# Kernel optimization log

Measured on AMD Instinct MI355X. Metric: run time of the kernel, lower is better.

Reference implementation:

```python
import jax, jax.numpy as jnp
import numpy as np

B, LQ, LK, D, H = 8, 1024, 1024, 1024, 16
HD = D // H  # 64


def setup_inputs() -> dict:
    key = jax.random.key(0)
    ks = jax.random.split(key, 8)
    s = 0.02  # weight init scale
    return {
        "q_in": jax.random.normal(ks[0], (B, LQ, D), jnp.float32),
        "k_in": jax.random.normal(ks[1], (B, LK, D), jnp.float32),
        "v_in": jax.random.normal(ks[2], (B, LK, D), jnp.float32),
        "wq": jax.random.normal(ks[3], (D, D), jnp.float32) * s,
        "bq": jnp.zeros((D,), jnp.float32),
        "wk": jax.random.normal(ks[4], (D, D), jnp.float32) * s,
        "bk": jnp.zeros((D,), jnp.float32),
        "wv": jax.random.normal(ks[5], (D, D), jnp.float32) * s,
        "bv": jnp.zeros((D,), jnp.float32),
        "wo": jax.random.normal(ks[6], (D, D), jnp.float32) * s,
        "bo": jnp.zeros((D,), jnp.float32),
        # is_masked=True buffer: tril of ones -> True on lower triangle (masked-out positions, per original masked_fill semantics)
        "mask": jnp.tril(jnp.ones((LQ, LK), jnp.bool_)),
    }


def reference(q_in, k_in, v_in, wq, bq, wk, bk, wv, bv, wo, bo, mask):
    # torch Linear: x @ W.T + b
    q = (q_in @ wq.T + bq).reshape(B, H, LQ, HD)  # plain view, as in original
    k = (k_in @ wk.T + bk).reshape(B, H, LK, HD)
    v = (v_in @ wv.T + bv).reshape(B, H, LK, HD)
    # QUIRK: original scales by sqrt(query.size(1)) == sqrt(head_num), not sqrt(head_dim)
    scale = jnp.sqrt(jnp.float32(H))
    h = jnp.einsum("bhik,bhjk->bhij", q, k) / scale  # [B,H,LQ,LK]
    # masked_fill(-inf) then nan_to_num (maps -inf -> finfo.min, matching torch defaults)
    h = jnp.nan_to_num(jnp.where(mask, -jnp.inf, h))
    w = jax.nn.softmax(h, axis=-1)
    heads = jnp.einsum("bhij,bhjv->bhiv", w, v).reshape(B, LQ, H * HD)
    return heads @ wo.T + bo
```

## Files before the change

kernel.cpp:

```cpp
#include <hip/hip_runtime.h>
#include <hip/hip_bf16.h>

typedef __bf16 bf16;
typedef _Float16 f16;
typedef __attribute__((ext_vector_type(8))) __bf16 bf16x8;
typedef __attribute__((ext_vector_type(4))) __bf16 bf16x4;
typedef __attribute__((ext_vector_type(8))) _Float16 f16x8;
typedef __attribute__((ext_vector_type(4))) _Float16 f16x4;
typedef __attribute__((ext_vector_type(4))) float f32x4;

#define BB 8
#define SEQ 1024
#define DD 1024
#define HDIM 64
#define CHUNK 65536
#define MROWS (BB * SEQ)
#define NE_IN 8388608
#define NE_W  1048576

#define QSCALE 0.3606737602222409f

__device__ __forceinline__ void async_load16(const bf16* g, bf16* l) {
  __builtin_amdgcn_global_load_lds(
      (const __attribute__((address_space(1))) void*)g,
      (__attribute__((address_space(3))) void*)l, 16, 0, 0);
}

struct CvtArgs {
  const float* src[7];
  bf16* dst[7];
  int n[7];
};
__global__ __launch_bounds__(256) void cvt_bf16(CvtArgs a) {
  const int t = blockIdx.y;
  const long idx = ((long)blockIdx.x * 256 + threadIdx.x) * 8;
  if (idx >= a.n[t]) return;
  const float* s = a.src[t] + idx;
  f32x4 x = *(const f32x4*)s;
  f32x4 y = *(const f32x4*)(s + 4);
  bf16x8 o;
  o[0] = (bf16)x[0]; o[1] = (bf16)x[1]; o[2] = (bf16)x[2]; o[3] = (bf16)x[3];
  o[4] = (bf16)y[0]; o[5] = (bf16)y[1]; o[6] = (bf16)y[2]; o[7] = (bf16)y[3];
  *(bf16x8*)(a.dst[t] + idx) = o;
}

__global__ __launch_bounds__(256) void gemm_qkv(
    const bf16* __restrict__ Abase, const bf16* __restrict__ Wbase,
    const float* __restrict__ bq, const float* __restrict__ bk,
    const float* __restrict__ bv, bf16* __restrict__ Obase)
{
  __shared__ __attribute__((aligned(16))) bf16 As[128 * 32];
  __shared__ __attribute__((aligned(16))) bf16 Bs[128 * 32];

  const int tid  = threadIdx.x;
  const int lane = tid & 63;
  const int wid  = tid >> 6;
  const int wm   = wid >> 1, wn = wid & 1;
  const int quad = lane >> 4, l15 = lane & 15;
  const int m0 = blockIdx.x * 128;
  const int n0 = blockIdx.y * 128;
  const int t  = n0 >> 10;

  const bf16* A = Abase + (size_t)t * NE_IN;
  const float* bias = (t == 0) ? bq : (t == 1) ? bk : bv;
  const float scale = (t == 0) ? QSCALE : 1.0f;
  bf16* Cout = Obase + (size_t)t * NE_IN;
  const int nc0 = n0 & 1023;

  f32x4 acc[4][4];
#pragma unroll
  for (int i = 0; i < 4; i++)
#pragma unroll
    for (int j = 0; j < 4; j++) acc[i][j] = f32x4{0.f, 0.f, 0.f, 0.f};

  const int srow = wid * 16 + (lane >> 2);
  const int scol = (lane & 3) * 8;
  const bf16* gA = A + (size_t)(m0 + srow) * DD + scol;
  const bf16* gB = Wbase + (size_t)(n0 + srow) * DD + scol;
  bf16* lA = As + wid * 512;
  bf16* lB = Bs + wid * 512;

  for (int k0 = 0; k0 < DD; k0 += 32) {
    async_load16(gA + k0,           lA);
    async_load16(gA + k0 + 64 * DD, lA + 2048);
    async_load16(gB + k0,           lB);
    async_load16(gB + k0 + 64 * DD, lB + 2048);
    __syncthreads();

    bf16x8 af[4], bfr[4];
#pragma unroll
    for (int mi = 0; mi < 4; mi++)
      af[mi] = *(const bf16x8*)&As[(wm * 64 + mi * 16 + l15) * 32 + quad * 8];
#pragma unroll
    for (int ni = 0; ni < 4; ni++)
      bfr[ni] = *(const bf16x8*)&Bs[(wn * 64 + ni * 16 + l15) * 32 + quad * 8];
#pragma unroll
    for (int mi = 0; mi < 4; mi++)
#pragma unroll
      for (int ni = 0; ni < 4; ni++)
        acc[mi][ni] = __builtin_amdgcn_mfma_f32_16x16x32_bf16(
            af[mi], bfr[ni], acc[mi][ni], 0, 0, 0);
    __syncthreads();
  }

#pragma unroll
  for (int mi = 0; mi < 4; mi++) {
#pragma unroll
    for (int ni = 0; ni < 4; ni++) {
      const int col = nc0 + wn * 64 + ni * 16 + l15;
      const float bv_ = bias[col];
#pragma unroll
      for (int r = 0; r < 4; r++) {
        const int row = m0 + wm * 64 + mi * 16 + quad * 4 + r;
        Cout[(size_t)row * DD + col] = (bf16)((acc[mi][ni][r] + bv_) * scale);
      }
    }
  }
}

__global__ __launch_bounds__(256) void gemm_out(
    const bf16* __restrict__ A, const bf16* __restrict__ Bw,
    const float* __restrict__ bias, float* __restrict__ Cout)
{
  __shared__ __attribute__((aligned(16))) bf16 As[128 * 32];
  __shared__ __attribute__((aligned(16))) bf16 Bs[128 * 32];

  const int tid  = threadIdx.x;
  const int lane = tid & 63;
  const int wid  = tid >> 6;
  const int wm   = wid >> 1, wn = wid & 1;
  const int quad = lane >> 4, l15 = lane & 15;
  const int m0 = blockIdx.x * 128;
  const int n0 = blockIdx.y * 128;

  f32x4 acc[4][4];
#pragma unroll
  for (int i = 0; i < 4; i++)
#pragma unroll
    for (int j = 0; j < 4; j++) acc[i][j] = f32x4{0.f, 0.f, 0.f, 0.f};

  const int srow = wid * 16 + (lane >> 2);
  const int scol = (lane & 3) * 8;
  const bf16* gA = A  + (size_t)(m0 + srow) * DD + scol;
  const bf16* gB = Bw + (size_t)(n0 + srow) * DD + scol;
  bf16* lA = As + wid * 512;
  bf16* lB = Bs + wid * 512;

  for (int k0 = 0; k0 < DD; k0 += 32) {
    async_load16(gA + k0,           lA);
    async_load16(gA + k0 + 64 * DD, lA + 2048);
    async_load16(gB + k0,           lB);
    async_load16(gB + k0 + 64 * DD, lB + 2048);
    __syncthreads();

    bf16x8 af[4], bfr[4];
#pragma unroll
    for (int mi = 0; mi < 4; mi++)
      af[mi] = *(const bf16x8*)&As[(wm * 64 + mi * 16 + l15) * 32 + quad * 8];
#pragma unroll
    for (int ni = 0; ni < 4; ni++)
      bfr[ni] = *(const bf16x8*)&Bs[(wn * 64 + ni * 16 + l15) * 32 + quad * 8];
#pragma unroll
    for (int mi = 0; mi < 4; mi++)
#pragma unroll
      for (int ni = 0; ni < 4; ni++)
        acc[mi][ni] = __builtin_amdgcn_mfma_f32_16x16x32_bf16(
            af[mi], bfr[ni], acc[mi][ni], 0, 0, 0);
    __syncthreads();
  }

#pragma unroll
  for (int mi = 0; mi < 4; mi++) {
#pragma unroll
    for (int ni = 0; ni < 4; ni++) {
      const int col = n0 + wn * 64 + ni * 16 + l15;
      const float bv_ = bias[col];
#pragma unroll
      for (int r = 0; r < 4; r++) {
        const int row = m0 + wm * 64 + mi * 16 + quad * 4 + r;
        Cout[(size_t)row * DD + col] = acc[mi][ni][r] + bv_;
      }
    }
  }
}

__global__ __launch_bounds__(256) void vtrans(
    const bf16* __restrict__ V, f16* __restrict__ Vt)
{
  __shared__ __attribute__((aligned(16))) bf16 T[64][72];
  const int tid = threadIdx.x;
  const int r  = tid >> 2;
  const int c0 = (tid & 3) * 16;
  const size_t base = (size_t)blockIdx.y * CHUNK;
  const int kv0 = blockIdx.x * 64;

  const bf16* src = V + base + (size_t)(kv0 + r) * HDIM + c0;
  *(bf16x8*)&T[r][c0]     = *(const bf16x8*)src;
  *(bf16x8*)&T[r][c0 + 8] = *(const bf16x8*)(src + 8);
  __syncthreads();

  f16x8 o0, o1;
#pragma unroll
  for (int j = 0; j < 8; j++) {
    o0[j] = (f16)(float)T[c0 + j][r];
    o1[j] = (f16)(float)T[c0 + 8 + j][r];
  }
  f16* dst = Vt + base + (size_t)r * SEQ + kv0 + c0;
  *(f16x8*)dst       = o0;
  *(f16x8*)(dst + 8) = o1;
}

__global__ __launch_bounds__(256) void attn6(
    const bf16* __restrict__ Q, const bf16* __restrict__ K,
    const f16* __restrict__ Vt, bf16* __restrict__ O)
{
  __shared__ __attribute__((aligned(16))) bf16 Ks[64][72];
  __shared__ __attribute__((aligned(16))) f16  Vs[64][72];

  const int tid  = threadIdx.x;
  const int lane = tid & 63;
  const int wid  = tid >> 6;
  const int quad = lane >> 4, l15 = lane & 15;
  const int q0   = blockIdx.y * 128;
  const size_t base = (size_t)blockIdx.x * CHUNK;

  const int sA = q0 + wid * 16;
  const int sB = sA + 64;
  const int qgA = sA + l15;
  const int qgB = sB + l15;

  bf16x8 qbA[2], qbB[2];
#pragma unroll
  for (int ks = 0; ks < 2; ks++) {
    qbA[ks] = *(const bf16x8*)&Q[base + (size_t)qgA * HDIM + ks * 32 + quad * 8];
    qbB[ks] = *(const bf16x8*)&Q[base + (size_t)qgB * HDIM + ks * 32 + quad * 8];
  }

  f32x4 oaccA[4], oaccB[4], laccA, laccB;
#pragma unroll
  for (int h = 0; h < 4; h++) {
    oaccA[h] = f32x4{0.f, 0.f, 0.f, 0.f};
    oaccB[h] = f32x4{0.f, 0.f, 0.f, 0.f};
  }
  laccA = f32x4{0.f, 0.f, 0.f, 0.f};
  laccB = f32x4{0.f, 0.f, 0.f, 0.f};
  const f16x4 ones = f16x4{(f16)1.f, (f16)1.f, (f16)1.f, (f16)1.f};

  const int sr = tid >> 2;
  const int sc = (tid & 3) * 16;
  const bf16* gK = K  + base + (size_t)sr * HDIM + sc;
  const f16*  gV = Vt + base + (size_t)sr * SEQ  + sc;

  const bool lastBlk = (q0 == SEQ - 128);
  const int kv_begin = lastBlk ? 0 : q0;
  const bool uniRow = lastBlk && (wid == 3);

  for (int kv0 = kv_begin; kv0 < SEQ; kv0 += 64) {
    {
      const bf16* pk = gK + (size_t)kv0 * HDIM;
      *(bf16x8*)&Ks[sr][sc]     = *(const bf16x8*)pk;
      *(bf16x8*)&Ks[sr][sc + 8] = *(const bf16x8*)(pk + 8);
      const f16* pv = gV + kv0;
      *(f16x8*)&Vs[sr][sc]     = *(const f16x8*)pv;
      *(f16x8*)&Vs[sr][sc + 8] = *(const f16x8*)(pv + 8);
    }
    __syncthreads();

    const bool activeA = (kv0 + 63 > sA);
    const bool activeB = (kv0 + 63 > sB);

#pragma unroll
    for (int t = 0; t < 4; t++) {
      bf16x8 kf0 = *(const bf16x8*)&Ks[t * 16 + l15][quad * 8];
      bf16x8 kf1 = *(const bf16x8*)&Ks[t * 16 + l15][32 + quad * 8];
      f16x4 vf[4];
#pragma unroll
      for (int h = 0; h < 4; h++)
        vf[h] = *(const f16x4*)&Vs[h * 16 + l15][t * 16 + quad * 4];

      if (activeA) {
        f32x4 s = f32x4{0.f, 0.f, 0.f, 0.f};
        s = __builtin_amdgcn_mfma_f32_16x16x32_bf16(kf0, qbA[0], s, 0, 0, 0);
        s = __builtin_amdgcn_mfma_f32_16x16x32_bf16(kf1, qbA[1], s, 0, 0, 0);
        f16x4 pf;
        if (kv0 + t * 16 <= sA + 15) {
#pragma unroll
          for (int r = 0; r < 4; r++) {
            const int kvg = kv0 + t * 16 + quad * 4 + r;
            const float p = (kvg <= qgA) ? 0.f : __builtin_amdgcn_exp2f(s[r]);
            pf[r] = (f16)p;
          }
        } else {
#pragma unroll
          for (int r = 0; r < 4; r++) pf[r] = (f16)__builtin_amdgcn_exp2f(s[r]);
        }
        laccA = __builtin_amdgcn_mfma_f32_16x16x16f16(ones, pf, laccA, 0, 0, 0);
#pragma unroll
        for (int h = 0; h < 4; h++)
          oaccA[h] = __builtin_amdgcn_mfma_f32_16x16x16f16(vf[h], pf, oaccA[h], 0, 0, 0);
      }

      if (activeB) {
        f32x4 s = f32x4{0.f, 0.f, 0.f, 0.f};
        s = __builtin_amdgcn_mfma_f32_16x16x32_bf16(kf0, qbB[0], s, 0, 0, 0);
        s = __builtin_amdgcn_mfma_f32_16x16x32_bf16(kf1, qbB[1], s, 0, 0, 0);
        f16x4 pf;
        if (kv0 + t * 16 <= sB + 15) {
#pragma unroll
          for (int r = 0; r < 4; r++) {
            const int kvg = kv0 + t * 16 + quad * 4 + r;
            const float p = (kvg <= qgB) ? ((qgB == SEQ - 1) ? 1.f : 0.f)
                                         : __builtin_amdgcn_exp2f(s[r]);
            pf[r] = (f16)p;
          }
        } else {
#pragma unroll
          for (int r = 0; r < 4; r++) pf[r] = (f16)__builtin_amdgcn_exp2f(s[r]);
        }
        laccB = __builtin_amdgcn_mfma_f32_16x16x16f16(ones, pf, laccB, 0, 0, 0);
#pragma unroll
        for (int h = 0; h < 4; h++)
          oaccB[h] = __builtin_amdgcn_mfma_f32_16x16x16f16(vf[h], pf, oaccB[h], 0, 0, 0);
      } else if (uniRow) {
        f16x4 pf = (l15 == 15) ? ones : f16x4{(f16)0.f, (f16)0.f, (f16)0.f, (f16)0.f};
        laccB = __builtin_amdgcn_mfma_f32_16x16x16f16(ones, pf, laccB, 0, 0, 0);
#pragma unroll
        for (int h = 0; h < 4; h++)
          oaccB[h] = __builtin_amdgcn_mfma_f32_16x16x16f16(vf[h], pf, oaccB[h], 0, 0, 0);
      }
    }
    __syncthreads();
  }

  const float rinvA = 1.0f / laccA[0];
  const float rinvB = 1.0f / laccB[0];

#pragma unroll
  for (int h = 0; h < 4; h++) {
    bf16x4 w;
#pragma unroll
    for (int r = 0; r < 4; r++) w[r] = (bf16)(oaccA[h][r] * rinvA);
    *(bf16x4*)&Ks[wid * 16 + l15][h * 16 + quad * 4] = w;
  }
  __syncthreads();
  {
    const int row = tid >> 2;
    const int c   = (tid & 3) * 16;
    bf16* dst = O + base + (size_t)(q0 + row) * HDIM + c;
    *(bf16x8*)dst       = *(const bf16x8*)&Ks[row][c];
    *(bf16x8*)(dst + 8) = *(const bf16x8*)&Ks[row][c + 8];
  }
  __syncthreads();
#pragma unroll
  for (int h = 0; h < 4; h++) {
    bf16x4 w;
#pragma unroll
    for (int r = 0; r < 4; r++) w[r] = (bf16)(oaccB[h][r] * rinvB);
    *(bf16x4*)&Ks[wid * 16 + l15][h * 16 + quad * 4] = w;
  }
  __syncthreads();
  {
    const int row = tid >> 2;
    const int c   = (tid & 3) * 16;
    bf16* dst = O + base + (size_t)(q0 + 64 + row) * HDIM + c;
    *(bf16x8*)dst       = *(const bf16x8*)&Ks[row][c];
    *(bf16x8*)(dst + 8) = *(const bf16x8*)&Ks[row][c + 8];
  }
}

extern "C" void kernel_launch(void* const* d_in, const int* in_sizes, int n_in,
                              void* d_out, int out_size, void* d_ws, size_t ws_size,
                              hipStream_t stream) {
  (void)in_sizes; (void)n_in; (void)out_size; (void)ws_size;
  const float* q_in = (const float*)d_in[0];
  const float* k_in = (const float*)d_in[1];
  const float* v_in = (const float*)d_in[2];
  const float* wq   = (const float*)d_in[3];
  const float* bq   = (const float*)d_in[4];
  const float* wk   = (const float*)d_in[5];
  const float* bk   = (const float*)d_in[6];
  const float* wv   = (const float*)d_in[7];
  const float* bv   = (const float*)d_in[8];
  const float* wo   = (const float*)d_in[9];
  const float* bo   = (const float*)d_in[10];

  bf16* wqb  = (bf16*)d_ws;
  bf16* wkb  = wqb + NE_W;
  bf16* wvb  = wkb + NE_W;
  bf16* wob  = wvb + NE_W;
  bf16* qinb = wob + NE_W;
  bf16* kinb = qinb + NE_IN;
  bf16* vinb = kinb + NE_IN;
  bf16* Qb   = vinb + NE_IN;
  bf16* Kb   = Qb + NE_IN;
  bf16* Vb   = Kb + NE_IN;
  f16*  VtG  = (f16*)qinb;
  bf16* Hb   = kinb;

  CvtArgs ca;
  ca.src[0] = q_in; ca.dst[0] = qinb; ca.n[0] = NE_IN;
  ca.src[1] = k_in; ca.dst[1] = kinb; ca.n[1] = NE_IN;
  ca.src[2] = v_in; ca.dst[2] = vinb; ca.n[2] = NE_IN;
  ca.src[3] = wq;   ca.dst[3] = wqb;  ca.n[3] = NE_W;
  ca.src[4] = wk;   ca.dst[4] = wkb;  ca.n[4] = NE_W;
  ca.src[5] = wv;   ca.dst[5] = wvb;  ca.n[5] = NE_W;
  ca.src[6] = wo;   ca.dst[6] = wob;  ca.n[6] = NE_W;
  cvt_bf16<<<dim3(NE_IN / 2048, 7), 256, 0, stream>>>(ca);

  gemm_qkv<<<dim3(MROWS / 128, 3 * DD / 128), 256, 0, stream>>>(
      qinb, wqb, bq, bk, bv, Qb);

  vtrans<<<dim3(SEQ / 64, BB * 16), 256, 0, stream>>>(Vb, VtG);
  attn6<<<dim3(BB * 16, SEQ / 128), 256, 0, stream>>>(Qb, Kb, VtG, Hb);

  gemm_out<<<dim3(MROWS / 128, DD / 128), 256, 0, stream>>>(
      Hb, wob, bo, (float*)d_out);
}
```

Measured before the change: 311.9 us.

## Rewrite QKV GEMM as 256x256 8-wave multi-stage pipelined kernel

The QKV projection GEMM moves from 128x128 tiles with 4 waves and a single LDS buffer to 256x256 tiles with 8 waves and a 128KB double-buffered LDS ring. Async global-to-LDS loads are issued several phases ahead, with explicit vmcnt waits, raw barriers and setprio around the MFMA bursts. A block-index swizzle is added to group tiles for L2 reuse. This is meant to hide load latency and cut LDS and global traffic per FLOP, at the cost of lower occupancy, a large LDS footprint and fragile hand-tuned wait counts.

```diff
diff --git a/kernel.cpp b/kernel.cpp
--- a/kernel.cpp
+++ b/kernel.cpp
@@ -44,74 +44,131 @@
   *(bf16x8*)(a.dst[t] + idx) = o;
 }
 
-__global__ __launch_bounds__(256) void gemm_qkv(
+
+__device__ __forceinline__ void stage_u(int u, const bf16* gA, const bf16* gB,
+                                        bf16* lds, int sdst) {
+  if (u < 64) {
+    const int t_  = u >> 2;
+    const int kh_ = (u >> 1) & 1;
+    const bf16* g_ = ((u & 1) ? gB : gA) + t_ * 64 + kh_ * 32;
+    bf16* l_ = lds + ((t_ & 1) << 15) + ((u & 1) << 14) + (kh_ << 13) + sdst;
+    async_load16(g_, l_);
+    async_load16(g_ + 128 * 1024, l_ + 4096);
+  }
+}
+
+template <int N>
+__device__ __forceinline__ void vmwait() {
+  if constexpr (N >= 0)
+    asm volatile("s_waitcnt vmcnt(%0)" ::"n"(N) : "memory");
+}
+
+template <int BUF, int KH, int MH, bool RDB, int VM>
+__device__ __forceinline__ void phase8(bf16* lds, int aoff, int boff, int u,
+                                       const bf16* gA, const bf16* gB,
+                                       int sdst, f32x4 (&acc)[8][4],
+                                       bf16x8 (&bfr)[4]) {
+  const bf16* ab = lds + BUF * 32768 + KH * 8192 + MH * 2048 + aoff;
+  bf16x8 af[4];
+#pragma unroll
+  for (int f = 0; f < 4; f++) af[f] = *(const bf16x8*)(ab + f * 512);
+  if constexpr (RDB) {
+    const bf16* bb = lds + BUF * 32768 + 16384 + KH * 8192 + boff;
+#pragma unroll
+    for (int f = 0; f < 4; f++) bfr[f] = *(const bf16x8*)(bb + f * 512);
+  }
+  stage_u(u, gA, gB, lds, sdst);
+  __builtin_amdgcn_s_barrier();
+  __builtin_amdgcn_s_setprio(1);
+#pragma unroll
+  for (int f = 0; f < 4; f++)
+#pragma unroll
+    for (int ni = 0; ni < 4; ni++)
+      acc[MH * 4 + f][ni] = __builtin_amdgcn_mfma_f32_16x16x32_bf16(
+          af[f], bfr[ni], acc[MH * 4 + f][ni], 0, 0, 0);
+  __builtin_amdgcn_s_setprio(0);
+  asm volatile("s_waitcnt lgkmcnt(0)" ::: "memory");
+  vmwait<VM>();
+  __builtin_amdgcn_s_barrier();
+}
+
+template <int VM1, int VM3, int VM5, int VM7>
+__device__ __forceinline__ void iter8(bf16* lds, int aoff, int boff, int ub,
+                                      const bf16* gA, const bf16* gB, int sdst,
+                                      f32x4 (&acc)[8][4], bf16x8 (&bfr)[4]) {
+  phase8<0, 0, 0, true,  -1 >(lds, aoff, boff, ub + 6,  gA, gB, sdst, acc, bfr);
+  phase8<0, 0, 1, false, VM1>(lds, aoff, boff, ub + 7,  gA, gB, sdst, acc, bfr);
+  phase8<0, 1, 0, true,  -1 >(lds, aoff, boff, ub + 8,  gA, gB, sdst, acc, bfr);
+  phase8<0, 1, 1, false, VM3>(lds, aoff, boff, ub + 9,  gA, gB, sdst, acc, bfr);
+  phase8<1, 0, 0, true,  -1 >(lds, aoff, boff, ub + 10, gA, gB, sdst, acc, bfr);
+  phase8<1, 0, 1, false, VM5>(lds, aoff, boff, ub + 11, gA, gB, sdst, acc, bfr);
+  phase8<1, 1, 0, true,  -1 >(lds, aoff, boff, ub + 12, gA, gB, sdst, acc, bfr);
+  phase8<1, 1, 1, false, VM7>(lds, aoff, boff, ub + 13, gA, gB, sdst, acc, bfr);
+}
+
+__global__ __launch_bounds__(512, 2) void gemm_qkv8(
     const bf16* __restrict__ Abase, const bf16* __restrict__ Wbase,
     const float* __restrict__ bq, const float* __restrict__ bk,
     const float* __restrict__ bv, bf16* __restrict__ Obase)
 {
-  __shared__ __attribute__((aligned(16))) bf16 As[128 * 32];
-  __shared__ __attribute__((aligned(16))) bf16 Bs[128 * 32];
+  __shared__ __attribute__((aligned(16))) bf16 lds[65536];
 
   const int tid  = threadIdx.x;
   const int lane = tid & 63;
   const int wid  = tid >> 6;
-  const int wm   = wid >> 1, wn = wid & 1;
+  const int wm   = wid >> 2, wn = wid & 3;
   const int quad = lane >> 4, l15 = lane & 15;
-  const int m0 = blockIdx.x * 128;
-  const int n0 = blockIdx.y * 128;
-  const int t  = n0 >> 10;
+
+  const int bid  = blockIdx.x;
+  const int wg   = (bid & 7) * 48 + (bid >> 3);
+  const int mblk = wg / 12, nblk = wg % 12;
+  const int m0   = mblk * 256;
+  const int n0g  = nblk * 256;
+  const int t    = n0g >> 10;
+  const int n0   = n0g & 1023;
 
   const bf16* A = Abase + (size_t)t * NE_IN;
+  const bf16* B = Wbase + (size_t)t * NE_W;
   const float* bias = (t == 0) ? bq : (t == 1) ? bk : bv;
   const float scale = (t == 0) ? QSCALE : 1.0f;
   bf16* Cout = Obase + (size_t)t * NE_IN;
-  const int nc0 = n0 & 1023;
-
-  f32x4 acc[4][4];
-#pragma unroll
-  for (int i = 0; i < 4; i++)
+
+  const int srow = tid >> 2;
+  const int scol = (tid & 3) * 8;
+  const bf16* gA = A + (size_t)(m0 + srow) * DD + scol;
+  const bf16* gB = B + (size_t)(n0 + srow) * DD + scol;
+  const int sdst = wid << 9;
+
+  const int aoff = (wm * 128 + l15) * 32 + quad * 8;
+  const int boff = (wn * 64 + l15) * 32 + quad * 8;
+
+  f32x4 acc[8][4];
+#pragma unroll
+  for (int i = 0; i < 8; i++)
 #pragma unroll
     for (int j = 0; j < 4; j++) acc[i][j] = f32x4{0.f, 0.f, 0.f, 0.f};
-
-  const int srow = wid * 16 + (lane >> 2);
-  const int scol = (lane & 3) * 8;
-  const bf16* gA = A + (size_t)(m0 + srow) * DD + scol;
-  const bf16* gB = Wbase + (size_t)(n0 + srow) * DD + scol;
-  bf16* lA = As + wid * 512;
-  bf16* lB = Bs + wid * 512;
-
-  for (int k0 = 0; k0 < DD; k0 += 32) {
-    async_load16(gA + k0,           lA);
-    async_load16(gA + k0 + 64 * DD, lA + 2048);
-    async_load16(gB + k0,           lB);
-    async_load16(gB + k0 + 64 * DD, lB + 2048);
-    __syncthreads();
-
-    bf16x8 af[4], bfr[4];
-#pragma unroll
-    for (int mi = 0; mi < 4; mi++)
-      af[mi] = *(const bf16x8*)&As[(wm * 64 + mi * 16 + l15) * 32 + quad * 8];
-#pragma unroll
-    for (int ni = 0; ni < 4; ni++)
-      bfr[ni] = *(const bf16x8*)&Bs[(wn * 64 + ni * 16 + l15) * 32 + quad * 8];
-#pragma unroll
-    for (int mi = 0; mi < 4; mi++)
-#pragma unroll
-      for (int ni = 0; ni < 4; ni++)
-        acc[mi][ni] = __builtin_amdgcn_mfma_f32_16x16x32_bf16(
-            af[mi], bfr[ni], acc[mi][ni], 0, 0, 0);
-    __syncthreads();
-  }
-
-#pragma unroll
-  for (int mi = 0; mi < 4; mi++) {
+  bf16x8 bfr[4];
+
+#pragma unroll
+  for (int u = 0; u < 6; ++u) stage_u(u, gA, gB, lds, sdst);
+  asm volatile("s_waitcnt vmcnt(8)" ::: "memory");
+  __builtin_amdgcn_s_barrier();
+
+#pragma unroll 1
+  for (int i = 0; i < 7; ++i)
+    iter8<8, 8, 8, 8>(lds, aoff, boff, 8 * i, gA, gB, sdst, acc, bfr);
+  iter8<8, 4, 0, -1>(lds, aoff, boff, 56, gA, gB, sdst, acc, bfr);
+
+  const int col0 = n0 + wn * 64;
+#pragma unroll
+  for (int mi = 0; mi < 8; mi++) {
 #pragma unroll
     for (int ni = 0; ni < 4; ni++) {
-      const int col = nc0 + wn * 64 + ni * 16 + l15;
+      const int col = col0 + ni * 16 + l15;
       const float bv_ = bias[col];
 #pragma unroll
       for (int r = 0; r < 4; r++) {
-        const int row = m0 + wm * 64 + mi * 16 + quad * 4 + r;
+        const int row = m0 + wm * 128 + mi * 16 + quad * 4 + r;
         Cout[(size_t)row * DD + col] = (bf16)((acc[mi][ni][r] + bv_) * scale);
       }
     }
@@ -407,8 +464,7 @@
   ca.src[6] = wo;   ca.dst[6] = wob;  ca.n[6] = NE_W;
   cvt_bf16<<<dim3(NE_IN / 2048, 7), 256, 0, stream>>>(ca);
 
-  gemm_qkv<<<dim3(MROWS / 128, 3 * DD / 128), 256, 0, stream>>>(
-      qinb, wqb, bq, bk, bv, Qb);
+  gemm_qkv8<<<dim3(384), 512, 0, stream>>>(qinb, wqb, bq, bk, bv, Qb);
 
   vtrans<<<dim3(SEQ / 64, BB * 16), 256, 0, stream>>>(Vb, VtG);
   attn6<<<dim3(BB * 16, SEQ / 128), 256, 0, stream>>>(Qb, Kb, VtG, Hb);
```

Measured after the change: 317.9 us. About the same (+1.9%).

## Fuse fp32-to-bf16 activation conversion into QKV GEMM A-tile loads

Applied to the files above, without the earlier changes.

The separate conversion of the three large fp32 activation inputs to bf16 is removed. The QKV GEMM now loads fp32 A tiles directly into registers, converts them in-kernel and writes bf16 to LDS, prefetching the next k-slice into registers. This saves a full write and re-read of the bf16 activation copies. In exchange, the GEMM re-reads fp32 activations once per N tile (8 times per input), doubling A-side global traffic, and it gives up asynchronous global-to-LDS loads for A.

```diff
diff --git a/kernel.cpp b/kernel.cpp
--- a/kernel.cpp
+++ b/kernel.cpp
@@ -26,26 +26,29 @@
       (__attribute__((address_space(3))) void*)l, 16, 0, 0);
 }
 
+__device__ __forceinline__ bf16x8 cvt8(f32x4 x, f32x4 y) {
+  bf16x8 o;
+  o[0] = (bf16)x[0]; o[1] = (bf16)x[1]; o[2] = (bf16)x[2]; o[3] = (bf16)x[3];
+  o[4] = (bf16)y[0]; o[5] = (bf16)y[1]; o[6] = (bf16)y[2]; o[7] = (bf16)y[3];
+  return o;
+}
+
 struct CvtArgs {
-  const float* src[7];
-  bf16* dst[7];
-  int n[7];
+  const float* src[4];
+  bf16* dst[4];
 };
 __global__ __launch_bounds__(256) void cvt_bf16(CvtArgs a) {
   const int t = blockIdx.y;
   const long idx = ((long)blockIdx.x * 256 + threadIdx.x) * 8;
-  if (idx >= a.n[t]) return;
   const float* s = a.src[t] + idx;
   f32x4 x = *(const f32x4*)s;
   f32x4 y = *(const f32x4*)(s + 4);
-  bf16x8 o;
-  o[0] = (bf16)x[0]; o[1] = (bf16)x[1]; o[2] = (bf16)x[2]; o[3] = (bf16)x[3];
-  o[4] = (bf16)y[0]; o[5] = (bf16)y[1]; o[6] = (bf16)y[2]; o[7] = (bf16)y[3];
-  *(bf16x8*)(a.dst[t] + idx) = o;
+  *(bf16x8*)(a.dst[t] + idx) = cvt8(x, y);
 }
 
 __global__ __launch_bounds__(256) void gemm_qkv(
-    const bf16* __restrict__ Abase, const bf16* __restrict__ Wbase,
+    const float* __restrict__ Aq, const float* __restrict__ Ak,
+    const float* __restrict__ Av, const bf16* __restrict__ Wbase,
     const float* __restrict__ bq, const float* __restrict__ bk,
     const float* __restrict__ bv, bf16* __restrict__ Obase)
 {
@@ -61,7 +64,7 @@
   const int n0 = blockIdx.y * 128;
   const int t  = n0 >> 10;
 
-  const bf16* A = Abase + (size_t)t * NE_IN;
+  const float* Af = (t == 0) ? Aq : (t == 1) ? Ak : Av;
   const float* bias = (t == 0) ? bq : (t == 1) ? bk : bv;
   const float scale = (t == 0) ? QSCALE : 1.0f;
   bf16* Cout = Obase + (size_t)t * NE_IN;
@@ -75,17 +78,31 @@
 
   const int srow = wid * 16 + (lane >> 2);
   const int scol = (lane & 3) * 8;
-  const bf16* gA = A + (size_t)(m0 + srow) * DD + scol;
-  const bf16* gB = Wbase + (size_t)(n0 + srow) * DD + scol;
-  bf16* lA = As + wid * 512;
+  const float* gAf = Af + (size_t)(m0 + srow) * DD + scol;
+  const bf16*  gB  = Wbase + (size_t)(n0 + srow) * DD + scol;
   bf16* lB = Bs + wid * 512;
+  bf16* wA0 = As + srow * 32 + scol;
+  bf16* wA1 = wA0 + 64 * 32;
+
+  f32x4 a0 = *(const f32x4*)(gAf);
+  f32x4 a1 = *(const f32x4*)(gAf + 4);
+  f32x4 a2 = *(const f32x4*)(gAf + (size_t)64 * DD);
+  f32x4 a3 = *(const f32x4*)(gAf + (size_t)64 * DD + 4);
 
   for (int k0 = 0; k0 < DD; k0 += 32) {
-    async_load16(gA + k0,           lA);
-    async_load16(gA + k0 + 64 * DD, lA + 2048);
+    *(bf16x8*)wA0 = cvt8(a0, a1);
+    *(bf16x8*)wA1 = cvt8(a2, a3);
     async_load16(gB + k0,           lB);
     async_load16(gB + k0 + 64 * DD, lB + 2048);
     __syncthreads();
+
+    if (k0 + 32 < DD) {
+      const float* p = gAf + k0 + 32;
+      a0 = *(const f32x4*)(p);
+      a1 = *(const f32x4*)(p + 4);
+      a2 = *(const f32x4*)(p + (size_t)64 * DD);
+      a3 = *(const f32x4*)(p + (size_t)64 * DD + 4);
+    }
 
     bf16x8 af[4], bfr[4];
 #pragma unroll
@@ -398,17 +415,14 @@
   bf16* Hb   = kinb;
 
   CvtArgs ca;
-  ca.src[0] = q_in; ca.dst[0] = qinb; ca.n[0] = NE_IN;
-  ca.src[1] = k_in; ca.dst[1] = kinb; ca.n[1] = NE_IN;
-  ca.src[2] = v_in; ca.dst[2] = vinb; ca.n[2] = NE_IN;
-  ca.src[3] = wq;   ca.dst[3] = wqb;  ca.n[3] = NE_W;
-  ca.src[4] = wk;   ca.dst[4] = wkb;  ca.n[4] = NE_W;
-  ca.src[5] = wv;   ca.dst[5] = wvb;  ca.n[5] = NE_W;
-  ca.src[6] = wo;   ca.dst[6] = wob;  ca.n[6] = NE_W;
-  cvt_bf16<<<dim3(NE_IN / 2048, 7), 256, 0, stream>>>(ca);
+  ca.src[0] = wq; ca.dst[0] = wqb;
+  ca.src[1] = wk; ca.dst[1] = wkb;
+  ca.src[2] = wv; ca.dst[2] = wvb;
+  ca.src[3] = wo; ca.dst[3] = wob;
+  cvt_bf16<<<dim3(NE_W / 2048, 4), 256, 0, stream>>>(ca);
 
   gemm_qkv<<<dim3(MROWS / 128, 3 * DD / 128), 256, 0, stream>>>(
-      qinb, wqb, bq, bk, bv, Qb);
+      q_in, k_in, v_in, wqb, bq, bk, bv, Qb);
 
   vtrans<<<dim3(SEQ / 64, BB * 16), 256, 0, stream>>>(Vb, VtG);
   attn6<<<dim3(BB * 16, SEQ / 128), 256, 0, stream>>>(Qb, Kb, VtG, Hb);
```

Result: slower. 318.7 us (+2.2%).

## Triple-buffer LDS tiles in projection GEMMs with async prefetch two stages ahead

Applied to the files above, without the earlier changes.

Both the QKV and output projection GEMMs now keep three LDS buffers per operand and issue async global-to-LDS loads two k-steps ahead of the MFMA compute. Hand-written s_waitcnt/s_barrier sequences replace the two __syncthreads per iteration with a single barrier that waits only for the oldest tile. The aim is to hide global load latency behind the MFMA work. In exchange, LDS use per block triples, which may reduce occupancy, and correctness depends on the hand-counted vmcnt values.

```diff
diff --git a/kernel.cpp b/kernel.cpp
--- a/kernel.cpp
+++ b/kernel.cpp
@@ -44,13 +44,44 @@
   *(bf16x8*)(a.dst[t] + idx) = o;
 }
 
+__device__ __forceinline__ void stage_tile(const bf16* gA, const bf16* gB,
+                                           bf16* lA, bf16* lB, int k0) {
+  async_load16(gA + k0,           lA);
+  async_load16(gA + k0 + 64 * DD, lA + 2048);
+  async_load16(gB + k0,           lB);
+  async_load16(gB + k0 + 64 * DD, lB + 2048);
+}
+
+__device__ __forceinline__ void mfma_tile(const bf16* Asb, const bf16* Bsb,
+                                          int wm, int wn, int quad, int l15,
+                                          f32x4 (&acc)[4][4]) {
+  bf16x8 af[4], bfr[4];
+#pragma unroll
+  for (int mi = 0; mi < 4; mi++)
+    af[mi] = *(const bf16x8*)&Asb[(wm * 64 + mi * 16 + l15) * 32 + quad * 8];
+#pragma unroll
+  for (int ni = 0; ni < 4; ni++)
+    bfr[ni] = *(const bf16x8*)&Bsb[(wn * 64 + ni * 16 + l15) * 32 + quad * 8];
+#pragma unroll
+  for (int mi = 0; mi < 4; mi++)
+#pragma unroll
+    for (int ni = 0; ni < 4; ni++)
+      acc[mi][ni] = __builtin_amdgcn_mfma_f32_16x16x32_bf16(
+          af[mi], bfr[ni], acc[mi][ni], 0, 0, 0);
+}
+
+#define GEMM_SYNC(N)                                                     \
+  asm volatile("s_waitcnt lgkmcnt(0)\n\t"                                \
+               "s_waitcnt vmcnt(" #N ")\n\t"                             \
+               "s_barrier" ::: "memory")
+
 __global__ __launch_bounds__(256) void gemm_qkv(
     const bf16* __restrict__ Abase, const bf16* __restrict__ Wbase,
     const float* __restrict__ bq, const float* __restrict__ bk,
     const float* __restrict__ bv, bf16* __restrict__ Obase)
 {
-  __shared__ __attribute__((aligned(16))) bf16 As[128 * 32];
-  __shared__ __attribute__((aligned(16))) bf16 Bs[128 * 32];
+  __shared__ __attribute__((aligned(16))) bf16 As[3][4096];
+  __shared__ __attribute__((aligned(16))) bf16 Bs[3][4096];
 
   const int tid  = threadIdx.x;
   const int lane = tid & 63;
@@ -77,31 +108,22 @@
   const int scol = (lane & 3) * 8;
   const bf16* gA = A + (size_t)(m0 + srow) * DD + scol;
   const bf16* gB = Wbase + (size_t)(n0 + srow) * DD + scol;
-  bf16* lA = As + wid * 512;
-  bf16* lB = Bs + wid * 512;
-
-  for (int k0 = 0; k0 < DD; k0 += 32) {
-    async_load16(gA + k0,           lA);
-    async_load16(gA + k0 + 64 * DD, lA + 2048);
-    async_load16(gB + k0,           lB);
-    async_load16(gB + k0 + 64 * DD, lB + 2048);
-    __syncthreads();
-
-    bf16x8 af[4], bfr[4];
-#pragma unroll
-    for (int mi = 0; mi < 4; mi++)
-      af[mi] = *(const bf16x8*)&As[(wm * 64 + mi * 16 + l15) * 32 + quad * 8];
-#pragma unroll
-    for (int ni = 0; ni < 4; ni++)
-      bfr[ni] = *(const bf16x8*)&Bs[(wn * 64 + ni * 16 + l15) * 32 + quad * 8];
-#pragma unroll
-    for (int mi = 0; mi < 4; mi++)
-#pragma unroll
-      for (int ni = 0; ni < 4; ni++)
-        acc[mi][ni] = __builtin_amdgcn_mfma_f32_16x16x32_bf16(
-            af[mi], bfr[ni], acc[mi][ni], 0, 0, 0);
-    __syncthreads();
-  }
+  const int sl = wid * 512;
+
+  stage_tile(gA, gB, &As[0][sl], &Bs[0][sl], 0);
+  stage_tile(gA, gB, &As[1][sl], &Bs[1][sl], 32);
+  asm volatile("s_waitcnt vmcnt(4)\n\ts_barrier" ::: "memory");
+
+#pragma unroll 3
+  for (int it = 0; it < 30; ++it) {
+    const int bw = (it + 2) % 3;
+    stage_tile(gA, gB, &As[bw][sl], &Bs[bw][sl], (it + 2) * 32);
+    mfma_tile(&As[it % 3][0], &Bs[it % 3][0], wm, wn, quad, l15, acc);
+    GEMM_SYNC(4);
+  }
+  mfma_tile(&As[0][0], &Bs[0][0], wm, wn, quad, l15, acc);
+  GEMM_SYNC(0);
+  mfma_tile(&As[1][0], &Bs[1][0], wm, wn, quad, l15, acc);
 
 #pragma unroll
   for (int mi = 0; mi < 4; mi++) {
@@ -122,8 +144,8 @@
     const bf16* __restrict__ A, const bf16* __restrict__ Bw,
     const float* __restrict__ bias, float* __restrict__ Cout)
 {
-  __shared__ __attribute__((aligned(16))) bf16 As[128 * 32];
-  __shared__ __attribute__((aligned(16))) bf16 Bs[128 * 32];
+  __shared__ __attribute__((aligned(16))) bf16 As[3][4096];
+  __shared__ __attribute__((aligned(16))) bf16 Bs[3][4096];
 
   const int tid  = threadIdx.x;
   const int lane = tid & 63;
@@ -143,31 +165,22 @@
   const int scol = (lane & 3) * 8;
   const bf16* gA = A  + (size_t)(m0 + srow) * DD + scol;
   const bf16* gB = Bw + (size_t)(n0 + srow) * DD + scol;
-  bf16* lA = As + wid * 512;
-  bf16* lB = Bs + wid * 512;
-
-  for (int k0 = 0; k0 < DD; k0 += 32) {
-    async_load16(gA + k0,           lA);
-    async_load16(gA + k0 + 64 * DD, lA + 2048);
-    async_load16(gB + k0,           lB);
-    async_load16(gB + k0 + 64 * DD, lB + 2048);
-    __syncthreads();
-
-    bf16x8 af[4], bfr[4];
-#pragma unroll
-    for (int mi = 0; mi < 4; mi++)
-      af[mi] = *(const bf16x8*)&As[(wm * 64 + mi * 16 + l15) * 32 + quad * 8];
-#pragma unroll
-    for (int ni = 0; ni < 4; ni++)
-      bfr[ni] = *(const bf16x8*)&Bs[(wn * 64 + ni * 16 + l15) * 32 + quad * 8];
-#pragma unroll
-    for (int mi = 0; mi < 4; mi++)
-#pragma unroll
-      for (int ni = 0; ni < 4; ni++)
-        acc[mi][ni] = __builtin_amdgcn_mfma_f32_16x16x32_bf16(
-            af[mi], bfr[ni], acc[mi][ni], 0, 0, 0);
-    __syncthreads();
-  }
+  const int sl = wid * 512;
+
+  stage_tile(gA, gB, &As[0][sl], &Bs[0][sl], 0);
+  stage_tile(gA, gB, &As[1][sl], &Bs[1][sl], 32);
+  asm volatile("s_waitcnt vmcnt(4)\n\ts_barrier" ::: "memory");
+
+#pragma unroll 3
+  for (int it = 0; it < 30; ++it) {
+    const int bw = (it + 2) % 3;
+    stage_tile(gA, gB, &As[bw][sl], &Bs[bw][sl], (it + 2) * 32);
+    mfma_tile(&As[it % 3][0], &Bs[it % 3][0], wm, wn, quad, l15, acc);
+    GEMM_SYNC(4);
+  }
+  mfma_tile(&As[0][0], &Bs[0][0], wm, wn, quad, l15, acc);
+  GEMM_SYNC(0);
+  mfma_tile(&As[1][0], &Bs[1][0], wm, wn, quad, l15, acc);
 
 #pragma unroll
   for (int mi = 0; mi < 4; mi++) {
```

After: 321.3 us. +3.0%, slower.
